# Performance work log

Measured on AMD Instinct MI355X. Metric: run time of the kernel, lower is better.

The kernel has to match this reference:

```python
import jax, jax.numpy as jnp
import numpy as np

HEAD = 4

def setup_inputs() -> dict:
    key = jax.random.key(0)
    ks = jax.random.split(key, 6)
    n_nodes = 100000
    n_edges = 1600000
    latdim = 128
    embeds = jax.random.normal(ks[0], (n_nodes, latdim), dtype=jnp.float32)
    qTrans = jax.random.normal(ks[1], (latdim, latdim), dtype=jnp.float32) * (1.0 / np.sqrt(latdim))
    kTrans = jax.random.normal(ks[2], (latdim, latdim), dtype=jnp.float32) * (1.0 / np.sqrt(latdim))
    vTrans = jax.random.normal(ks[3], (latdim, latdim), dtype=jnp.float32) * (1.0 / np.sqrt(latdim))
    rows = jax.random.randint(ks[4], (n_edges,), 0, n_nodes, dtype=jnp.int64) if jax.config.jax_enable_x64 else jax.random.randint(ks[4], (n_edges,), 0, n_nodes, dtype=jnp.int32)
    cols = jax.random.randint(ks[5], (n_edges,), 0, n_nodes, dtype=rows.dtype)
    return {"embeds": embeds, "qTrans": qTrans, "kTrans": kTrans, "vTrans": vTrans,
            "rows": rows, "cols": cols, "n_nodes": n_nodes}


def reference(embeds, qTrans, kTrans, vTrans, rows, cols, n_nodes):
    latdim = embeds.shape[1]
    dh = latdim // HEAD  # per-head dim
    # Gather endpoint embeddings per edge: [E, latdim]
    rowEmbeds = embeds[rows]
    colEmbeds = embeds[cols]
    # Per-edge QKV projections reshaped to [E, H, dh]
    q = (rowEmbeds @ qTrans).reshape(-1, HEAD, dh)
    k = (colEmbeds @ kTrans).reshape(-1, HEAD, dh)
    v = (colEmbeds @ vTrans).reshape(-1, HEAD, dh)
    # Per-edge, per-head attention logits
    att = jnp.einsum('ehd,ehd->eh', q, k)
    att = jnp.clip(att, -10.0, 10.0)
    expAtt = jnp.exp(att)
    # Segmented softmax normalization over destination nodes (rows)
    attNorm = jax.ops.segment_sum(expAtt, rows, num_segments=n_nodes)[rows]
    att = expAtt / (attNorm + 1e-8)
    # Weight values and scatter-add back to nodes
    resEdges = (att[:, :, None] * v).reshape(-1, latdim)
    resEmbeds = jax.ops.segment_sum(resEdges, rows, num_segments=n_nodes)
    return resEmbeds, att
```

## Files before the change

kernel.cpp:

```cpp
#include <hip/hip_runtime.h>

#define LAT 128
#define CAP 256

__global__ __launch_bounds__(256) void proj_kernel(
    const float* __restrict__ A,
    const float* __restrict__ Wq, const float* __restrict__ Wk, const float* __restrict__ Wv,
    float* __restrict__ Cq, float* __restrict__ Ckv,
    int N)
{
  __shared__ float eL[64][132];
  __shared__ float wL[64][132];
  const int t = threadIdx.x;
  const int n0 = blockIdx.x * 64;
  const int mat = blockIdx.y;
  const float* W = (mat == 0) ? Wq : (mat == 1) ? Wk : Wv;

  #pragma unroll
  for (int it = 0; it < 8; ++it) {
    int flat = (it * 256 + t) * 4;
    int n = flat >> 7, kk = flat & 127;
    float4 v = make_float4(0.f, 0.f, 0.f, 0.f);
    if (n0 + n < N) v = *(const float4*)(A + (size_t)(n0 + n) * LAT + kk);
    *(float4*)&eL[n][kk] = v;
  }

  const int nl = t & 15;
  const int j0 = t >> 4;
  float acc[4][8] = {};

  for (int kt = 0; kt < 2; ++kt) {
    __syncthreads();
    #pragma unroll
    for (int it = 0; it < 8; ++it) {
      int flat = (it * 256 + t) * 4;
      int kk = flat >> 7, c = flat & 127;
      *(float4*)&wL[kk][c] = *(const float4*)(W + (size_t)(kt * 64 + kk) * LAT + c);
    }
    __syncthreads();
    #pragma unroll 2
    for (int kk = 0; kk < 64; kk += 2) {
      float4 wa0 = *(float4*)&wL[kk][j0 * 4];
      float4 wb0 = *(float4*)&wL[kk][64 + j0 * 4];
      float4 wa1 = *(float4*)&wL[kk + 1][j0 * 4];
      float4 wb1 = *(float4*)&wL[kk + 1][64 + j0 * 4];
      #pragma unroll
      for (int i = 0; i < 4; ++i) {
        float2 e = *(float2*)&eL[nl + 16 * i][kt * 64 + kk];
        acc[i][0] += e.x * wa0.x + e.y * wa1.x;
        acc[i][1] += e.x * wa0.y + e.y * wa1.y;
        acc[i][2] += e.x * wa0.z + e.y * wa1.z;
        acc[i][3] += e.x * wa0.w + e.y * wa1.w;
        acc[i][4] += e.x * wb0.x + e.y * wb1.x;
        acc[i][5] += e.x * wb0.y + e.y * wb1.y;
        acc[i][6] += e.x * wb0.z + e.y * wb1.z;
        acc[i][7] += e.x * wb0.w + e.y * wb1.w;
      }
    }
  }

  #pragma unroll
  for (int i = 0; i < 4; ++i) {
    int n = n0 + nl + 16 * i;
    if (n < N) {
      float* C = (mat == 0) ? (Cq + (size_t)n * LAT)
                            : (Ckv + (size_t)n * 256 + (mat == 2 ? 128 : 0));
      *(float4*)(C + j0 * 4)      = make_float4(acc[i][0], acc[i][1], acc[i][2], acc[i][3]);
      *(float4*)(C + 64 + j0 * 4) = make_float4(acc[i][4], acc[i][5], acc[i][6], acc[i][7]);
    }
  }
}

__global__ __launch_bounds__(256) void deg_kernel(const int* __restrict__ rows,
                                                  int* __restrict__ counts, int E) {
  int i = blockIdx.x * 256 + threadIdx.x;
  if (i < E) atomicAdd(&counts[rows[i]], 1);
}

__global__ __launch_bounds__(1024) void scan1_kernel(const int* __restrict__ counts,
                                                     int* __restrict__ starts,
                                                     int* __restrict__ bsums, int N) {
  __shared__ int sh[1024];
  int t = threadIdx.x;
  int i = blockIdx.x * 1024 + t;
  int v = (i < N) ? counts[i] : 0;
  sh[t] = v; __syncthreads();
  for (int off = 1; off < 1024; off <<= 1) {
    int x = (t >= off) ? sh[t - off] : 0;
    __syncthreads();
    sh[t] += x;
    __syncthreads();
  }
  if (i < N) starts[i] = sh[t] - v;
  if (t == 1023) bsums[blockIdx.x] = sh[t];
}

__global__ __launch_bounds__(1024) void scan2_kernel(int* __restrict__ bsums, int nb) {
  __shared__ int sh[1024];
  int t = threadIdx.x;
  int v = (t < nb) ? bsums[t] : 0;
  sh[t] = v; __syncthreads();
  for (int off = 1; off < 1024; off <<= 1) {
    int x = (t >= off) ? sh[t - off] : 0;
    __syncthreads();
    sh[t] += x;
    __syncthreads();
  }
  if (t < nb) bsums[t] = sh[t] - v;
}

__global__ __launch_bounds__(256) void scan3_kernel(int* __restrict__ starts,
                                                    const int* __restrict__ bsums,
                                                    int* __restrict__ cursor, int N) {
  int i = blockIdx.x * 256 + threadIdx.x;
  if (i < N) {
    int s = starts[i] + bsums[i >> 10];
    starts[i] = s;
    cursor[i] = s;
  }
}

__global__ __launch_bounds__(256) void fill_kernel(const int* __restrict__ rows,
                                                   const int* __restrict__ cols,
                                                   int* __restrict__ cursor,
                                                   int* __restrict__ eidx,
                                                   int* __restrict__ ecol, int E) {
  int i = blockIdx.x * 256 + threadIdx.x;
  if (i < E) {
    int p = atomicAdd(&cursor[rows[i]], 1);
    eidx[p] = i;
    ecol[p] = cols[i];
  }
}

__global__ __launch_bounds__(256) void attn_kernel(
    const float* __restrict__ KV,
    const int* __restrict__ starts, const int* __restrict__ counts,
    const int* __restrict__ eidx, const int* __restrict__ ecol,
    float* __restrict__ outRes,
    float* __restrict__ outAtt,
    int N)
{
  __shared__ float eaL[4][CAP][4];
  const int w = threadIdx.x >> 6;
  const int lane = threadIdx.x & 63;
  const int n = blockIdx.x * 4 + w;
  if (n >= N) return;
  const int g = lane & 15;
  const int s = lane >> 4;
  const int start = starts[n];
  const int deg = counts[n];

  const float4 q0 = *(const float4*)(outRes + (size_t)n * LAT + g * 8);
  const float4 q1 = *(const float4*)(outRes + (size_t)n * LAT + g * 8 + 4);

  float denom = 0.f;
  float acc[8] = {};
  for (int base = 0; base < deg; base += 64) {
    int j = base + lane;
    int c_l = 0;
    if (j < deg) c_l = ecol[start + j];
    int m = deg - base; if (m > 64) m = 64;
    int steps = (m + 3) >> 2;
    #pragma unroll 2
    for (int st = 0; st < steps; ++st) {
      int jj = st * 4 + s;
      int c = __shfl(c_l, jj);
      bool valid = (jj < m);
      const float* kv = KV + (size_t)c * 256;
      float4 k0 = *(const float4*)(kv + g * 8);
      float4 k1 = *(const float4*)(kv + g * 8 + 4);
      float4 v0 = *(const float4*)(kv + 128 + g * 8);
      float4 v1 = *(const float4*)(kv + 128 + g * 8 + 4);
      float p = q0.x * k0.x + q0.y * k0.y + q0.z * k0.z + q0.w * k0.w
              + q1.x * k1.x + q1.y * k1.y + q1.z * k1.z + q1.w * k1.w;
      p += __shfl_xor(p, 1);
      p += __shfl_xor(p, 2);
      p = fminf(fmaxf(p, -10.f), 10.f);
      float ea = valid ? __expf(p) : 0.f;
      denom += ea;
      acc[0] += ea * v0.x; acc[1] += ea * v0.y; acc[2] += ea * v0.z; acc[3] += ea * v0.w;
      acc[4] += ea * v1.x; acc[5] += ea * v1.y; acc[6] += ea * v1.z; acc[7] += ea * v1.w;
      int idx = base + jj;
      if (valid && (g & 3) == 0 && idx < CAP) eaL[w][idx][g >> 2] = ea;
    }
  }
  denom += __shfl_xor(denom, 16);
  denom += __shfl_xor(denom, 32);
  #pragma unroll
  for (int i = 0; i < 8; ++i) {
    acc[i] += __shfl_xor(acc[i], 16);
    acc[i] += __shfl_xor(acc[i], 32);
  }
  const float rden = 1.f / (denom + 1e-8f);

  if (lane < 16) {
    float4 r0 = make_float4(acc[0] * rden, acc[1] * rden, acc[2] * rden, acc[3] * rden);
    float4 r1 = make_float4(acc[4] * rden, acc[5] * rden, acc[6] * rden, acc[7] * rden);
    *(float4*)(outRes + (size_t)n * LAT + g * 8) = r0;
    *(float4*)(outRes + (size_t)n * LAT + g * 8 + 4) = r1;
  }

  const float r0 = __shfl(rden, 0);
  const float r1 = __shfl(rden, 4);
  const float r2 = __shfl(rden, 8);
  const float r3 = __shfl(rden, 12);

  int capped = deg < CAP ? deg : CAP;
  for (int j = lane; j < capped; j += 64) {
    int e = eidx[start + j];
    float4 a = *(float4*)&eaL[w][j][0];
    a.x *= r0; a.y *= r1; a.z *= r2; a.w *= r3;
    *(float4*)(outAtt + (size_t)e * 4) = a;
  }

  const float myr = (g >> 2) == 0 ? r0 : (g >> 2) == 1 ? r1 : (g >> 2) == 2 ? r2 : r3;
  for (int base = CAP; base < deg; base += 64) {
    int j = base + lane;
    int c_l = 0, e_l = 0;
    if (j < deg) { c_l = ecol[start + j]; e_l = eidx[start + j]; }
    int m = deg - base; if (m > 64) m = 64;
    int steps = (m + 3) >> 2;
    for (int st = 0; st < steps; ++st) {
      int jj = st * 4 + s;
      int c = __shfl(c_l, jj);
      int e = __shfl(e_l, jj);
      bool valid = (jj < m);
      const float* kv = KV + (size_t)c * 256;
      float4 k0 = *(const float4*)(kv + g * 8);
      float4 k1 = *(const float4*)(kv + g * 8 + 4);
      float p = q0.x * k0.x + q0.y * k0.y + q0.z * k0.z + q0.w * k0.w
              + q1.x * k1.x + q1.y * k1.y + q1.z * k1.z + q1.w * k1.w;
      p += __shfl_xor(p, 1);
      p += __shfl_xor(p, 2);
      p = fminf(fmaxf(p, -10.f), 10.f);
      float av = __expf(p) * myr;
      int lb = lane & 48;
      float4 o;
      o.x = __shfl(av, lb + 0);
      o.y = __shfl(av, lb + 4);
      o.z = __shfl(av, lb + 8);
      o.w = __shfl(av, lb + 12);
      if (valid && g == 0) *(float4*)(outAtt + (size_t)e * 4) = o;
    }
  }
}

extern "C" void kernel_launch(void* const* d_in, const int* in_sizes, int n_in,
                              void* d_out, int out_size, void* d_ws, size_t ws_size,
                              hipStream_t stream) {
  const float* embeds = (const float*)d_in[0];
  const float* qT = (const float*)d_in[1];
  const float* kT = (const float*)d_in[2];
  const float* vT = (const float*)d_in[3];
  const int* rows = (const int*)d_in[4];
  const int* cols = (const int*)d_in[5];

  if (in_sizes[1] != LAT * LAT) return;
  const int N = in_sizes[0] / LAT;
  const int E = in_sizes[4];

  float* outRes = (float*)d_out;
  float* outAtt = outRes + (size_t)N * LAT;

  char* w = (char*)d_ws;
  size_t need = (size_t)N * 256 * 4 + (size_t)N * 4 * 3 + 1024 * 4 + (size_t)E * 4 * 2;
  if (ws_size < need) return;
  float* KV = (float*)w;      w += (size_t)N * 256 * 4;
  int* counts = (int*)w;      w += (size_t)N * 4;
  int* starts = (int*)w;      w += (size_t)N * 4;
  int* cursor = (int*)w;      w += (size_t)N * 4;
  int* bsums  = (int*)w;      w += 1024 * 4;
  int* eidx   = (int*)w;      w += (size_t)E * 4;
  int* ecol   = (int*)w;      w += (size_t)E * 4;

  hipMemsetAsync(counts, 0, (size_t)N * 4, stream);

  dim3 pg((N + 63) / 64, 3);
  proj_kernel<<<pg, 256, 0, stream>>>(embeds, qT, kT, vT, outRes, KV, N);

  deg_kernel<<<(E + 255) / 256, 256, 0, stream>>>(rows, counts, E);
  int nb = (N + 1023) / 1024;
  scan1_kernel<<<nb, 1024, 0, stream>>>(counts, starts, bsums, N);
  scan2_kernel<<<1, 1024, 0, stream>>>(bsums, nb);
  scan3_kernel<<<(N + 255) / 256, 256, 0, stream>>>(starts, bsums, cursor, N);
  fill_kernel<<<(E + 255) / 256, 256, 0, stream>>>(rows, cols, cursor, eidx, ecol, E);

  attn_kernel<<<(N + 3) / 4, 256, 0, stream>>>(KV, starts, counts, eidx, ecol,
                                               outRes, outAtt, N);
}
```

Measured before the change: 695.7 us.

## Use split-bf16 MFMA for node QKV projection

Replaces the FP32 FMA tiled projection GEMM with bf16 MFMA instructions. Each operand is split into high and low bf16 parts and three MFMAs per step emulate near-FP32 accuracy. A new prep kernel converts the weights into MFMA fragment layout once per call. The aim is to cut the compute time of the node projection, at the cost of some precision loss, an extra launch and 64KB of LDS per block.

```diff
diff --git a/kernel.cpp b/kernel.cpp
--- a/kernel.cpp
+++ b/kernel.cpp
@@ -3,70 +3,100 @@
 #define LAT 128
 #define CAP 256
 
+typedef __attribute__((ext_vector_type(8))) short bfrag;
+typedef __attribute__((ext_vector_type(4))) float f32x4;
+
+__device__ inline unsigned short f2bf(float f) {
+  unsigned u = __float_as_uint(f);
+  unsigned r = u + 0x7FFFu + ((u >> 16) & 1u);
+  return (unsigned short)(r >> 16);
+}
+
+__global__ __launch_bounds__(256) void wprep_kernel(
+    const float* __restrict__ Wq, const float* __restrict__ Wk, const float* __restrict__ Wv,
+    unsigned short* __restrict__ whi, unsigned short* __restrict__ wlo)
+{
+  int gid = blockIdx.x * 256 + threadIdx.x;
+  if (gid >= 3 * 16384) return;
+  int mat = gid >> 14;
+  int idx = gid & 16383;
+  int i = idx & 7;
+  int l = (idx >> 3) & 63;
+  int st = idx >> 9;
+  int k = (st >> 3) * 32 + ((l >> 4) << 3) + i;
+  int c = (st & 7) * 16 + (l & 15);
+  const float* W = (mat == 0) ? Wq : (mat == 1) ? Wk : Wv;
+  float f = W[k * LAT + c];
+  unsigned short h = f2bf(f);
+  float fh = __uint_as_float((unsigned)h << 16);
+  whi[gid] = h;
+  wlo[gid] = f2bf(f - fh);
+}
+
 __global__ __launch_bounds__(256) void proj_kernel(
     const float* __restrict__ A,
-    const float* __restrict__ Wq, const float* __restrict__ Wk, const float* __restrict__ Wv,
-    float* __restrict__ Cq, float* __restrict__ Ckv,
-    int N)
+    const unsigned short* __restrict__ whi, const unsigned short* __restrict__ wlo,
+    float* __restrict__ Cq, float* __restrict__ Ckv, int N)
 {
-  __shared__ float eL[64][132];
-  __shared__ float wL[64][132];
+  __shared__ unsigned short whiL[16384];
+  __shared__ unsigned short wloL[16384];
   const int t = threadIdx.x;
   const int n0 = blockIdx.x * 64;
   const int mat = blockIdx.y;
-  const float* W = (mat == 0) ? Wq : (mat == 1) ? Wk : Wv;
-
+  const unsigned short* wh = whi + mat * 16384;
+  const unsigned short* wl = wlo + mat * 16384;
   #pragma unroll
   for (int it = 0; it < 8; ++it) {
-    int flat = (it * 256 + t) * 4;
-    int n = flat >> 7, kk = flat & 127;
-    float4 v = make_float4(0.f, 0.f, 0.f, 0.f);
-    if (n0 + n < N) v = *(const float4*)(A + (size_t)(n0 + n) * LAT + kk);
-    *(float4*)&eL[n][kk] = v;
-  }
-
-  const int nl = t & 15;
-  const int j0 = t >> 4;
-  float acc[4][8] = {};
-
-  for (int kt = 0; kt < 2; ++kt) {
-    __syncthreads();
+    int o = (it * 256 + t) * 8;
+    *(float4*)&whiL[o] = *(const float4*)&wh[o];
+    *(float4*)&wloL[o] = *(const float4*)&wl[o];
+  }
+
+  const int w = t >> 6, lane = t & 63;
+  const int rowbase = n0 + w * 16;
+  int arow = rowbase + (lane & 15);
+  if (arow >= N) arow = N - 1;
+  const int khalf = lane >> 4;
+
+  bfrag Ah[4], Al[4];
+  #pragma unroll
+  for (int s = 0; s < 4; ++s) {
+    const float* ap = A + (size_t)arow * LAT + s * 32 + khalf * 8;
+    float4 x0 = *(const float4*)ap;
+    float4 x1 = *(const float4*)(ap + 4);
+    float xs[8] = {x0.x, x0.y, x0.z, x0.w, x1.x, x1.y, x1.z, x1.w};
     #pragma unroll
-    for (int it = 0; it < 8; ++it) {
-      int flat = (it * 256 + t) * 4;
-      int kk = flat >> 7, c = flat & 127;
-      *(float4*)&wL[kk][c] = *(const float4*)(W + (size_t)(kt * 64 + kk) * LAT + c);
-    }
-    __syncthreads();
-    #pragma unroll 2
-    for (int kk = 0; kk < 64; kk += 2) {
-      float4 wa0 = *(float4*)&wL[kk][j0 * 4];
-      float4 wb0 = *(float4*)&wL[kk][64 + j0 * 4];
-      float4 wa1 = *(float4*)&wL[kk + 1][j0 * 4];
-      float4 wb1 = *(float4*)&wL[kk + 1][64 + j0 * 4];
-      #pragma unroll
-      for (int i = 0; i < 4; ++i) {
-        float2 e = *(float2*)&eL[nl + 16 * i][kt * 64 + kk];
-        acc[i][0] += e.x * wa0.x + e.y * wa1.x;
-        acc[i][1] += e.x * wa0.y + e.y * wa1.y;
-        acc[i][2] += e.x * wa0.z + e.y * wa1.z;
-        acc[i][3] += e.x * wa0.w + e.y * wa1.w;
-        acc[i][4] += e.x * wb0.x + e.y * wb1.x;
-        acc[i][5] += e.x * wb0.y + e.y * wb1.y;
-        acc[i][6] += e.x * wb0.z + e.y * wb1.z;
-        acc[i][7] += e.x * wb0.w + e.y * wb1.w;
-      }
-    }
-  }
+    for (int i = 0; i < 8; ++i) {
+      unsigned short h = f2bf(xs[i]);
+      float fh = __uint_as_float((unsigned)h << 16);
+      Ah[s][i] = (short)h;
+      Al[s][i] = (short)f2bf(xs[i] - fh);
+    }
+  }
+  __syncthreads();
+
+  float* Cbase; int stride, cofs;
+  if (mat == 0) { Cbase = Cq;  stride = LAT; cofs = 0; }
+  else          { Cbase = Ckv; stride = 256; cofs = (mat == 2) ? 128 : 0; }
 
   #pragma unroll
-  for (int i = 0; i < 4; ++i) {
-    int n = n0 + nl + 16 * i;
-    if (n < N) {
-      float* C = (mat == 0) ? (Cq + (size_t)n * LAT)
-                            : (Ckv + (size_t)n * 256 + (mat == 2 ? 128 : 0));
-      *(float4*)(C + j0 * 4)      = make_float4(acc[i][0], acc[i][1], acc[i][2], acc[i][3]);
-      *(float4*)(C + 64 + j0 * 4) = make_float4(acc[i][4], acc[i][5], acc[i][6], acc[i][7]);
+  for (int tt = 0; tt < 8; ++tt) {
+    f32x4 acc = {0.f, 0.f, 0.f, 0.f};
+    #pragma unroll
+    for (int s = 0; s < 4; ++s) {
+      int o = ((s * 8 + tt) * 64 + lane) * 8;
+      bfrag bh = *(bfrag*)&whiL[o];
+      bfrag bl = *(bfrag*)&wloL[o];
+      acc = __builtin_amdgcn_mfma_f32_16x16x32_bf16(Ah[s], bh, acc, 0, 0, 0);
+      acc = __builtin_amdgcn_mfma_f32_16x16x32_bf16(Al[s], bh, acc, 0, 0, 0);
+      acc = __builtin_amdgcn_mfma_f32_16x16x32_bf16(Ah[s], bl, acc, 0, 0, 0);
+    }
+    int col = cofs + tt * 16 + (lane & 15);
+    int r0 = rowbase + (lane >> 4) * 4;
+    #pragma unroll
+    for (int r = 0; r < 4; ++r) {
+      int row = r0 + r;
+      if (row < N) Cbase[(size_t)row * stride + col] = acc[r];
     }
   }
 }
@@ -264,20 +294,23 @@
   float* outAtt = outRes + (size_t)N * LAT;
 
   char* w = (char*)d_ws;
-  size_t need = (size_t)N * 256 * 4 + (size_t)N * 4 * 3 + 1024 * 4 + (size_t)E * 4 * 2;
+  size_t need = (size_t)N * 1024 + (size_t)N * 12 + 4096 + (size_t)E * 8 + 2 * 98304;
   if (ws_size < need) return;
-  float* KV = (float*)w;      w += (size_t)N * 256 * 4;
-  int* counts = (int*)w;      w += (size_t)N * 4;
-  int* starts = (int*)w;      w += (size_t)N * 4;
-  int* cursor = (int*)w;      w += (size_t)N * 4;
-  int* bsums  = (int*)w;      w += 1024 * 4;
-  int* eidx   = (int*)w;      w += (size_t)E * 4;
-  int* ecol   = (int*)w;      w += (size_t)E * 4;
+  float* KV = (float*)w;            w += (size_t)N * 256 * 4;
+  int* counts = (int*)w;            w += (size_t)N * 4;
+  int* starts = (int*)w;            w += (size_t)N * 4;
+  int* cursor = (int*)w;            w += (size_t)N * 4;
+  int* bsums  = (int*)w;            w += 1024 * 4;
+  int* eidx   = (int*)w;            w += (size_t)E * 4;
+  int* ecol   = (int*)w;            w += (size_t)E * 4;
+  unsigned short* whi = (unsigned short*)w;  w += 3 * 16384 * 2;
+  unsigned short* wlo = (unsigned short*)w;  w += 3 * 16384 * 2;
 
   hipMemsetAsync(counts, 0, (size_t)N * 4, stream);
 
+  wprep_kernel<<<192, 256, 0, stream>>>(qT, kT, vT, whi, wlo);
   dim3 pg((N + 63) / 64, 3);
-  proj_kernel<<<pg, 256, 0, stream>>>(embeds, qT, kT, vT, outRes, KV, N);
+  proj_kernel<<<pg, 256, 0, stream>>>(embeds, whi, wlo, outRes, KV, N);
 
   deg_kernel<<<(E + 255) / 256, 256, 0, stream>>>(rows, counts, E);
   int nb = (N + 1023) / 1024;
```

New measurement: 590.1 us. -15.2%, faster.
